# Kernel tuning notes

Measured on AMD Instinct MI355X. Metric: run time of the kernel, lower is better.

## Reference

```python
import jax, jax.numpy as jnp
import numpy as np

N_TRAJ, T, D_DATA, D_LAT, N_UNITS = 8192, 100, 32, 64, 100

def setup_inputs() -> dict:
    key = jax.random.key(0)
    ks = jax.random.split(key, 12)
    w = lambda k, *shape: jax.random.normal(k, shape, jnp.float32) * 0.05
    z = lambda n: jnp.zeros((n,), jnp.float32)
    return {
        "data": jax.random.normal(ks[0], (N_TRAJ, T, D_DATA), jnp.float32),
        "time_steps": jnp.linspace(0.0, 1.0, T, dtype=jnp.float32),  # uniform grid -> dt < interval/50 always
        "prior": jax.random.normal(ks[1], (N_TRAJ, D_LAT), jnp.float32),
        # ODE func MLP: latent -> n_units -> latent
        "Wo1": w(ks[2], D_LAT, N_UNITS), "bo1": z(N_UNITS),
        "Wo2": w(ks[3], N_UNITS, D_LAT), "bo2": z(D_LAT),
        # GRU update/reset/candidate gates, each a 2-layer MLP on concat(y, x)
        "Wz1": w(ks[4], D_LAT + D_DATA, N_UNITS), "bz1": z(N_UNITS),
        "Wz2": w(ks[5], N_UNITS, D_LAT), "bz2": z(D_LAT),
        "Wr1": w(ks[6], D_LAT + D_DATA, N_UNITS), "br1": z(N_UNITS),
        "Wr2": w(ks[7], N_UNITS, D_LAT), "br2": z(D_LAT),
        "Wh1": w(ks[8], D_LAT + D_DATA, N_UNITS), "bh1": z(N_UNITS),
        "Wh2": w(ks[9], N_UNITS, D_LAT), "bh2": z(D_LAT),
    }

def _odernn(data, time_steps, prior,
            Wo1, bo1, Wo2, bo2,
            Wz1, bz1, Wz2, bz2,
            Wr1, br1, Wr2, br2,
            Wh1, bh1, Wh2, bh2):
    # Replicates the original loop's (prev_t, t_i) bookkeeping faithfully:
    # iteration 1 uses dt = ts[1] - ts[0]; after each iteration the code sets
    # prev_t, t_i = ts[i], ts[i-1], so iteration i >= 2 uses dt = ts[i-2] - ts[i-1].
    dts = jnp.concatenate([time_steps[1:2] - time_steps[0:1],
                           time_steps[:-2] - time_steps[1:-1]])  # [T-1]
    xs = jnp.swapaxes(data[:, 1:, :], 0, 1)  # [T-1, N, D_DATA] for scan

    def ode_func(y):  # [N, D_LAT] -> [N, D_LAT]
        return jnp.tanh(y @ Wo1 + bo1) @ Wo2 + bo2

    def gru_update(y, x):  # [N, D_LAT], [N, D_DATA] -> [N, D_LAT]
        yx = jnp.concatenate([y, x], axis=-1)
        zg = jax.nn.sigmoid(jnp.tanh(yx @ Wz1 + bz1) @ Wz2 + bz2)
        rg = jax.nn.sigmoid(jnp.tanh(yx @ Wr1 + br1) @ Wr2 + br2)
        ryx = jnp.concatenate([rg * y, x], axis=-1)
        h = jnp.tanh(jnp.tanh(ryx @ Wh1 + bh1) @ Wh2 + bh2)
        return (1.0 - zg) * h + zg * y

    def step(y, inp):
        dt, x = inp
        # |dt| < minimum_step branch: single explicit-Euler increment
        y_ode = y + ode_func(y) * dt
        return gru_update(y_ode, x), None

    y_final, _ = jax.lax.scan(step, prior, (dts, xs))
    return y_final

def reference(data, time_steps, prior,
              Wo1, bo1, Wo2, bo2,
              Wz1, bz1, Wz2, bz2,
              Wr1, br1, Wr2, br2,
              Wh1, bh1, Wh2, bh2):
    return _odernn(data, time_steps, prior,
                   Wo1, bo1, Wo2, bo2,
                   Wz1, bz1, Wz2, bz2,
                   Wr1, br1, Wr2, br2,
                   Wh1, bh1, Wh2, bh2)
```

## Files before the change

### kernel.cpp

```cpp
#include <hip/hip_runtime.h>

#define T_STEPS 100
#define NTRAJ   8192
#define MBLK    32
#define W_TILES 112
#define W_BYTES (W_TILES * 1024)
#define TILEBUF 22528
#define LDS_TOTAL (W_BYTES + 2 * TILEBUF)

typedef __attribute__((ext_vector_type(8))) _Float16 f16x8;
typedef __attribute__((ext_vector_type(4))) _Float16 f16x4;
typedef __attribute__((ext_vector_type(4))) float    f32x4;

#define MFMA16(a, b, c) __builtin_amdgcn_mfma_f32_16x16x32_f16((a), (b), (c), 0, 0, 0)

#define SWZ(row, col) ((col) ^ (((row) & 7) << 3))

__device__ __forceinline__ float fast_tanh(float x) {
    float e = __expf(2.f * x);
    return 1.f - 2.f * __builtin_amdgcn_rcpf(1.f + e);
}
__device__ __forceinline__ float fast_sigmoid(float x) {
    float e = __expf(-x);
    return __builtin_amdgcn_rcpf(1.f + e);
}

__global__ void pack_kernel(const float* __restrict__ Wo1, const float* __restrict__ Wo2,
                            const float* __restrict__ Wz1, const float* __restrict__ Wz2,
                            const float* __restrict__ Wr1, const float* __restrict__ Wr2,
                            const float* __restrict__ Wh1, const float* __restrict__ Wh2,
                            _Float16* __restrict__ P)
{
    int idx = blockIdx.x * 256 + threadIdx.x;
    if (idx >= 144 * 512) return;
    int tile = idx >> 9;
    int r    = idx & 511;
    int lane = r >> 3, j = r & 7;
    int krel = ((lane >> 4) << 3) + j;
    int c16  = lane & 15;
    float val = 0.f;

    if (tile < 14) {
        int t = tile, nt = t >> 1, kt = t & 1;
        int k = kt * 32 + krel, n = nt * 16 + c16;
        if (k < 64 && n < 100) val = Wo1[k * 100 + n];
    } else if (tile < 30) {
        int t = tile - 14, nt = t >> 2, kt = t & 3;
        int k = kt * 32 + krel, n = nt * 16 + c16;
        if (k < 100) val = Wo2[k * 64 + n];
    } else if (tile < 75) {
        int t = tile - 30, nt = t / 3, kt = t % 3;
        int k = kt * 32 + krel;
        if (nt < 7)      { int n = nt * 16 + c16;        if (n < 100) val = Wz1[k * 100 + n]; }
        else if (nt >= 8){ int n = (nt - 8) * 16 + c16;  if (n < 100) val = Wr1[k * 100 + n]; }
    } else if (tile < 107) {
        int t = tile - 75, gate = t >> 4, rem = t & 15, nt = rem >> 2, kt = rem & 3;
        int k = kt * 32 + krel, n = nt * 16 + c16;
        const float* W = gate ? Wr2 : Wz2;
        if (k < 100) val = W[k * 64 + n];
    } else if (tile < 128) {
        int t = tile - 107, nt = t / 3, kt = t % 3;
        int k = kt * 32 + krel, n = nt * 16 + c16;
        if (n < 100) val = Wh1[k * 100 + n];
    } else {
        int t = tile - 128, nt = t >> 2, kt = t & 3;
        int k = kt * 32 + krel, n = nt * 16 + c16;
        if (k < 100) val = Wh2[k * 64 + n];
    }
    P[idx] = (_Float16)val;
}

__device__ __forceinline__ f16x8 ldsA(const _Float16* buf, int stride, int row, int kcol) {
    return *(const f16x8*)(buf + row * stride + SWZ(row, kcol));
}
__device__ __forceinline__ void st4(_Float16* buf, int stride, int traj, int f0,
                                    float a, float b, float c, float d) {
    f16x4 h = {(_Float16)a, (_Float16)b, (_Float16)c, (_Float16)d};
    *(f16x4*)(buf + traj * stride + SWZ(traj, f0)) = h;
}
__device__ __forceinline__ f32x4 loadBias4(const float* b, int f0, int n) {
    f32x4 v = {0.f, 0.f, 0.f, 0.f};
    #pragma unroll
    for (int r = 0; r < 4; ++r) if (f0 + r < n) v[r] = b[f0 + r];
    return v;
}

__global__ __launch_bounds__(512, 2) void odernn_kernel(
    const float* __restrict__ data, const float* __restrict__ ts,
    const float* __restrict__ prior,
    const float* __restrict__ bo1, const float* __restrict__ bo2,
    const float* __restrict__ bz1, const float* __restrict__ bz2,
    const float* __restrict__ br1, const float* __restrict__ br2,
    const float* __restrict__ bh1, const float* __restrict__ bh2,
    const _Float16* __restrict__ P, float* __restrict__ out)
{
    extern __shared__ __align__(16) char smem[];
    _Float16* W = (_Float16*)smem;

    const int tid  = threadIdx.x;
    const int lane = tid & 63;
    const int wv   = tid >> 6;
    const int tg   = wv >> 2;
    const int wq   = wv & 3;
    const int c16  = lane & 15;
    const int g4   = lane >> 4;
    const int m0b  = blockIdx.x * MBLK;
    const int m0   = m0b + tg * 16;
    const int f0   = wq * 16 + (g4 << 2);
    const f16x8* Pt = (const f16x8*)P;
    const f16x8* Wv = (const f16x8*)W;

    _Float16* base = (_Float16*)(smem + W_BYTES + tg * TILEBUF);
    _Float16* sYb = base;
    _Float16* sYX = base + 1024;
    _Float16* sRX = base + 3072;
    _Float16* sH1 = base + 5120;
    _Float16* sZR = base + 7168;

    {
        f16x8* Wd = (f16x8*)W;
        #pragma unroll
        for (int it = 0; it < 14; ++it) {
            int idx = tid + it * 512;
            int ldst = idx >> 6, l = idx & 63;
            int srct = (ldst < 14) ? ldst : ldst + 16;
            Wd[idx] = Pt[srct * 64 + l];
        }
    }

    f32x4 bo1v[2], bh1v[2], bzrv[4];
    #pragma unroll
    for (int t = 0; t < 2; ++t) {
        int nt = wq + 4 * t;
        f32x4 zo = {0.f,0.f,0.f,0.f};
        if (nt < 7) {
            int ft = nt * 16 + (g4 << 2);
            bo1v[t] = loadBias4(bo1, ft, 100);
            bh1v[t] = loadBias4(bh1, ft, 100);
        } else { bo1v[t] = zo; bh1v[t] = zo; }
    }
    #pragma unroll
    for (int q = 0; q < 4; ++q) {
        int i = wq + 4 * q;
        f32x4 v = {0.f,0.f,0.f,0.f};
        if (i < 14) {
            int bt = (i < 7) ? i : i + 1;
            int ft = bt * 16 + (g4 << 2);
            if (i < 7) v = loadBias4(bz1, ft, 100);
            else       v = loadBias4(br1, ft - 128, 100);
        }
        bzrv[q] = v;
    }
    const f32x4 bo2v = *(const f32x4*)(bo2 + f0);
    const f32x4 bz2v = *(const f32x4*)(bz2 + f0);
    const f32x4 br2v = *(const f32x4*)(br2 + f0);
    const f32x4 bh2v = *(const f32x4*)(bh2 + f0);

    f16x8 Ao2[4], Ah2[4];
    #pragma unroll
    for (int kt = 0; kt < 4; ++kt) {
        Ao2[kt] = Pt[(14 + wq * 4 + kt) * 64 + lane];
        Ah2[kt] = Pt[(128 + wq * 4 + kt) * 64 + lane];
    }

    float y[4], yo[4] = {0,0,0,0}, zg[4] = {0,0,0,0};
    {
        f32x4 pv = *(const f32x4*)(prior + (size_t)(m0 + c16) * 64 + f0);
        #pragma unroll
        for (int r = 0; r < 4; ++r) y[r] = pv[r];
        st4(sYb, 64, c16, f0, y[0], y[1], y[2], y[3]);
    }
    {
        int row32 = tid >> 4, col = 112 + (tid & 15);
        int t = row32 >> 4, r16 = row32 & 15;
        _Float16* h1 = (_Float16*)(smem + W_BYTES + t * TILEBUF) + 5120;
        h1[r16 * 128 + SWZ(r16, col)] = (_Float16)0.f;
    }
    for (int i = tid; i < 2 * 16 * 32; i += 512) {
        int t = i >> 9, rem = i & 511;
        int r16 = rem >> 5, cc = rem & 31;
        int col = (cc < 16) ? (112 + cc) : (224 + cc);
        _Float16* zr = (_Float16*)(smem + W_BYTES + t * TILEBUF) + 7168;
        zr[r16 * 256 + SWZ(r16, col)] = (_Float16)0.f;
    }
    __syncthreads();

    const float t0v = ts[0], t1v = ts[1];

    const int t8 = tid & 255;
    const int rowA = t8 >> 5, xcol = t8 & 31;
    const int rowB = rowA + 8;
    const float* xpA = data + (size_t)(m0 + rowA) * (T_STEPS * 32) + 32 + xcol;
    const float* xpB = data + (size_t)(m0 + rowB) * (T_STEPS * 32) + 32 + xcol;
    const int xswA = rowA * 128 + SWZ(rowA, 64 + xcol);
    const int xswB = rowB * 128 + SWZ(rowB, 64 + xcol);
    float xvA = *xpA, xvB = *xpB;

    #pragma unroll 1
    for (int s = 0; s < T_STEPS - 1; ++s) {
        const float dt = (s == 0) ? (t1v - t0v) : (ts[s - 1] - ts[s]);

        {
            f16x8 b0 = ldsA(sYb, 64, c16, (g4 << 3));
            f16x8 b1 = ldsA(sYb, 64, c16, 32 + (g4 << 3));
            #pragma unroll
            for (int t = 0; t < 2; ++t) {
                int nt = wq + 4 * t;
                if (nt < 7) {
                    f32x4 acc0 = bo1v[t];
                    f32x4 z4 = {0.f, 0.f, 0.f, 0.f};
                    acc0 = MFMA16(Wv[(nt * 2 + 0) * 64 + lane], b0, acc0);
                    f32x4 acc1 = MFMA16(Wv[(nt * 2 + 1) * 64 + lane], b1, z4);
                    int ft = nt * 16 + (g4 << 2);
                    st4(sH1, 128, c16, ft,
                        fast_tanh(acc0[0] + acc1[0]), fast_tanh(acc0[1] + acc1[1]),
                        fast_tanh(acc0[2] + acc1[2]), fast_tanh(acc0[3] + acc1[3]));
                }
            }
        }
        {
            _Float16 a = (_Float16)xvA, b = (_Float16)xvB;
            sYX[xswA] = a; sRX[xswA] = a;
            sYX[xswB] = b; sRX[xswB] = b;
            xpA += 32; xpB += 32;
            if (s < T_STEPS - 2) { xvA = *xpA; xvB = *xpB; }
        }
        __syncthreads();

        {
            f32x4 acc0 = bo2v;
            f32x4 z4 = {0.f, 0.f, 0.f, 0.f};
            acc0 = MFMA16(Ao2[0], ldsA(sH1, 128, c16, 0 * 32 + (g4 << 3)), acc0);
            f32x4 acc1 = MFMA16(Ao2[1], ldsA(sH1, 128, c16, 1 * 32 + (g4 << 3)), z4);
            acc0 = MFMA16(Ao2[2], ldsA(sH1, 128, c16, 2 * 32 + (g4 << 3)), acc0);
            acc1 = MFMA16(Ao2[3], ldsA(sH1, 128, c16, 3 * 32 + (g4 << 3)), acc1);
            #pragma unroll
            for (int r = 0; r < 4; ++r) yo[r] = y[r] + dt * (acc0[r] + acc1[r]);
            st4(sYX, 128, c16, f0, yo[0], yo[1], yo[2], yo[3]);
        }
        __syncthreads();

        {
            f16x8 b0 = ldsA(sYX, 128, c16, 0 * 32 + (g4 << 3));
            f16x8 b1 = ldsA(sYX, 128, c16, 1 * 32 + (g4 << 3));
            f16x8 b2 = ldsA(sYX, 128, c16, 2 * 32 + (g4 << 3));
            #pragma unroll
            for (int q = 0; q < 4; ++q) {
                int i = wq + 4 * q;
                if (i < 14) {
                    int bt = (i < 7) ? i : i + 1;
                    f32x4 acc0 = bzrv[q];
                    f32x4 z4 = {0.f, 0.f, 0.f, 0.f};
                    acc0 = MFMA16(Wv[(14 + bt * 3 + 0) * 64 + lane], b0, acc0);
                    f32x4 acc1 = MFMA16(Wv[(14 + bt * 3 + 1) * 64 + lane], b1, z4);
                    acc0 = MFMA16(Wv[(14 + bt * 3 + 2) * 64 + lane], b2, acc0);
                    int ft = bt * 16 + (g4 << 2);
                    st4(sZR, 256, c16, ft,
                        fast_tanh(acc0[0] + acc1[0]), fast_tanh(acc0[1] + acc1[1]),
                        fast_tanh(acc0[2] + acc1[2]), fast_tanh(acc0[3] + acc1[3]));
                }
            }
        }
        __syncthreads();

        {
            f32x4 accz0 = bz2v, accr0 = br2v;
            f32x4 z4 = {0.f, 0.f, 0.f, 0.f};
            f32x4 accz1 = z4, accr1 = z4;
            accz0 = MFMA16(Wv[(59 + wq * 4 + 0) * 64 + lane], ldsA(sZR, 256, c16, 0 * 32 + (g4 << 3)), accz0);
            accr0 = MFMA16(Wv[(75 + wq * 4 + 0) * 64 + lane], ldsA(sZR, 256, c16, 128 + 0 * 32 + (g4 << 3)), accr0);
            accz1 = MFMA16(Wv[(59 + wq * 4 + 1) * 64 + lane], ldsA(sZR, 256, c16, 1 * 32 + (g4 << 3)), accz1);
            accr1 = MFMA16(Wv[(75 + wq * 4 + 1) * 64 + lane], ldsA(sZR, 256, c16, 128 + 1 * 32 + (g4 << 3)), accr1);
            accz0 = MFMA16(Wv[(59 + wq * 4 + 2) * 64 + lane], ldsA(sZR, 256, c16, 2 * 32 + (g4 << 3)), accz0);
            accr0 = MFMA16(Wv[(75 + wq * 4 + 2) * 64 + lane], ldsA(sZR, 256, c16, 128 + 2 * 32 + (g4 << 3)), accr0);
            accz1 = MFMA16(Wv[(59 + wq * 4 + 3) * 64 + lane], ldsA(sZR, 256, c16, 3 * 32 + (g4 << 3)), accz1);
            accr1 = MFMA16(Wv[(75 + wq * 4 + 3) * 64 + lane], ldsA(sZR, 256, c16, 128 + 3 * 32 + (g4 << 3)), accr1);
            float rv[4];
            #pragma unroll
            for (int r = 0; r < 4; ++r) {
                zg[r] = fast_sigmoid(accz0[r] + accz1[r]);
                rv[r] = fast_sigmoid(accr0[r] + accr1[r]) * yo[r];
            }
            st4(sRX, 128, c16, f0, rv[0], rv[1], rv[2], rv[3]);
        }
        __syncthreads();

        {
            f16x8 b0 = ldsA(sRX, 128, c16, 0 * 32 + (g4 << 3));
            f16x8 b1 = ldsA(sRX, 128, c16, 1 * 32 + (g4 << 3));
            f16x8 b2 = ldsA(sRX, 128, c16, 2 * 32 + (g4 << 3));
            #pragma unroll
            for (int t = 0; t < 2; ++t) {
                int nt = wq + 4 * t;
                if (nt < 7) {
                    f32x4 acc0 = bh1v[t];
                    f32x4 z4 = {0.f, 0.f, 0.f, 0.f};
                    acc0 = MFMA16(Wv[(91 + nt * 3 + 0) * 64 + lane], b0, acc0);
                    f32x4 acc1 = MFMA16(Wv[(91 + nt * 3 + 1) * 64 + lane], b1, z4);
                    acc0 = MFMA16(Wv[(91 + nt * 3 + 2) * 64 + lane], b2, acc0);
                    int ft = nt * 16 + (g4 << 2);
                    st4(sH1, 128, c16, ft,
                        fast_tanh(acc0[0] + acc1[0]), fast_tanh(acc0[1] + acc1[1]),
                        fast_tanh(acc0[2] + acc1[2]), fast_tanh(acc0[3] + acc1[3]));
                }
            }
        }
        __syncthreads();

        {
            f32x4 acc0 = bh2v;
            f32x4 z4 = {0.f, 0.f, 0.f, 0.f};
            acc0 = MFMA16(Ah2[0], ldsA(sH1, 128, c16, 0 * 32 + (g4 << 3)), acc0);
            f32x4 acc1 = MFMA16(Ah2[1], ldsA(sH1, 128, c16, 1 * 32 + (g4 << 3)), z4);
            acc0 = MFMA16(Ah2[2], ldsA(sH1, 128, c16, 2 * 32 + (g4 << 3)), acc0);
            acc1 = MFMA16(Ah2[3], ldsA(sH1, 128, c16, 3 * 32 + (g4 << 3)), acc1);
            #pragma unroll
            for (int r = 0; r < 4; ++r) {
                float h = fast_tanh(acc0[r] + acc1[r]);
                y[r] = (1.f - zg[r]) * h + zg[r] * yo[r];
            }
            st4(sYb, 64, c16, f0, y[0], y[1], y[2], y[3]);
        }
        __syncthreads();
    }

    {
        f32x4 ov = {y[0], y[1], y[2], y[3]};
        *(f32x4*)(out + (size_t)(m0 + c16) * 64 + f0) = ov;
    }
}

extern "C" void kernel_launch(void* const* d_in, const int* in_sizes, int n_in,
                              void* d_out, int out_size, void* d_ws, size_t ws_size,
                              hipStream_t stream) {
    const float* data = (const float*)d_in[0];
    const float* ts   = (const float*)d_in[1];
    const float* prior= (const float*)d_in[2];
    const float* Wo1 = (const float*)d_in[3];  const float* bo1 = (const float*)d_in[4];
    const float* Wo2 = (const float*)d_in[5];  const float* bo2 = (const float*)d_in[6];
    const float* Wz1 = (const float*)d_in[7];  const float* bz1 = (const float*)d_in[8];
    const float* Wz2 = (const float*)d_in[9];  const float* bz2 = (const float*)d_in[10];
    const float* Wr1 = (const float*)d_in[11]; const float* br1 = (const float*)d_in[12];
    const float* Wr2 = (const float*)d_in[13]; const float* br2 = (const float*)d_in[14];
    const float* Wh1 = (const float*)d_in[15]; const float* bh1 = (const float*)d_in[16];
    const float* Wh2 = (const float*)d_in[17]; const float* bh2 = (const float*)d_in[18];
    _Float16* P = (_Float16*)d_ws;
    float* out = (float*)d_out;

    hipFuncSetAttribute((const void*)odernn_kernel,
                        hipFuncAttributeMaxDynamicSharedMemorySize, LDS_TOTAL);

    hipLaunchKernelGGL(pack_kernel, dim3((144 * 512 + 255) / 256), dim3(256), 0, stream,
                       Wo1, Wo2, Wz1, Wz2, Wr1, Wr2, Wh1, Wh2, P);
    hipLaunchKernelGGL(odernn_kernel, dim3(NTRAJ / MBLK), dim3(512), LDS_TOTAL, stream,
                       data, ts, prior, bo1, bo2, bz1, bz2, br1, br2, bh1, bh2, P, out);
}
```

Before: 305.0 us.

## Feed data input as register MFMA fragment and precompute x-projections off critical path

Each lane now loads the next step's 8 data values straight into a register f16 fragment instead of staging them through LDS. The x-contributions to the z/r and h first-layer gates are computed early, during the ODE phase, as MFMA accumulators. The later gate MFMAs then chain from those partial sums and only read the 64-wide y or r*y tile from LDS. This shrinks the LDS tiles and takes one dependent MFMA off each serialized gate stage, at the cost of holding extra accumulator registers across barriers.

```diff
diff --git a/kernel.cpp b/kernel.cpp
--- a/kernel.cpp
+++ b/kernel.cpp
@@ -5,11 +5,12 @@
 #define MBLK    32
 #define W_TILES 112
 #define W_BYTES (W_TILES * 1024)
-#define TILEBUF 22528
+#define TILEBUF 18432
 #define LDS_TOTAL (W_BYTES + 2 * TILEBUF)
 
 typedef __attribute__((ext_vector_type(8))) _Float16 f16x8;
 typedef __attribute__((ext_vector_type(4))) _Float16 f16x4;
+typedef __attribute__((ext_vector_type(2))) __fp16   h16x2;
 typedef __attribute__((ext_vector_type(4))) float    f32x4;
 
 #define MFMA16(a, b, c) __builtin_amdgcn_mfma_f32_16x16x32_f16((a), (b), (c), 0, 0, 0)
@@ -84,6 +85,14 @@
     for (int r = 0; r < 4; ++r) if (f0 + r < n) v[r] = b[f0 + r];
     return v;
 }
+__device__ __forceinline__ f16x8 cvt8(f32x4 a, f32x4 b) {
+    union { h16x2 h2[4]; f16x8 v; } u;
+    u.h2[0] = __builtin_amdgcn_cvt_pkrtz(a[0], a[1]);
+    u.h2[1] = __builtin_amdgcn_cvt_pkrtz(a[2], a[3]);
+    u.h2[2] = __builtin_amdgcn_cvt_pkrtz(b[0], b[1]);
+    u.h2[3] = __builtin_amdgcn_cvt_pkrtz(b[2], b[3]);
+    return u.v;
+}
 
 __global__ __launch_bounds__(512, 2) void odernn_kernel(
     const float* __restrict__ data, const float* __restrict__ ts,
@@ -104,8 +113,7 @@
     const int wq   = wv & 3;
     const int c16  = lane & 15;
     const int g4   = lane >> 4;
-    const int m0b  = blockIdx.x * MBLK;
-    const int m0   = m0b + tg * 16;
+    const int m0   = blockIdx.x * MBLK + tg * 16;
     const int f0   = wq * 16 + (g4 << 2);
     const f16x8* Pt = (const f16x8*)P;
     const f16x8* Wv = (const f16x8*)W;
@@ -113,9 +121,9 @@
     _Float16* base = (_Float16*)(smem + W_BYTES + tg * TILEBUF);
     _Float16* sYb = base;
     _Float16* sYX = base + 1024;
-    _Float16* sRX = base + 3072;
-    _Float16* sH1 = base + 5120;
-    _Float16* sZR = base + 7168;
+    _Float16* sRX = base + 2048;
+    _Float16* sH1 = base + 3072;
+    _Float16* sZR = base + 5120;
 
     {
         f16x8* Wd = (f16x8*)W;
@@ -173,33 +181,35 @@
     {
         int row32 = tid >> 4, col = 112 + (tid & 15);
         int t = row32 >> 4, r16 = row32 & 15;
-        _Float16* h1 = (_Float16*)(smem + W_BYTES + t * TILEBUF) + 5120;
+        _Float16* h1 = (_Float16*)(smem + W_BYTES + t * TILEBUF) + 3072;
         h1[r16 * 128 + SWZ(r16, col)] = (_Float16)0.f;
     }
     for (int i = tid; i < 2 * 16 * 32; i += 512) {
         int t = i >> 9, rem = i & 511;
         int r16 = rem >> 5, cc = rem & 31;
         int col = (cc < 16) ? (112 + cc) : (224 + cc);
-        _Float16* zr = (_Float16*)(smem + W_BYTES + t * TILEBUF) + 7168;
+        _Float16* zr = (_Float16*)(smem + W_BYTES + t * TILEBUF) + 5120;
         zr[r16 * 256 + SWZ(r16, col)] = (_Float16)0.f;
     }
     __syncthreads();
 
     const float t0v = ts[0], t1v = ts[1];
 
-    const int t8 = tid & 255;
-    const int rowA = t8 >> 5, xcol = t8 & 31;
-    const int rowB = rowA + 8;
-    const float* xpA = data + (size_t)(m0 + rowA) * (T_STEPS * 32) + 32 + xcol;
-    const float* xpB = data + (size_t)(m0 + rowB) * (T_STEPS * 32) + 32 + xcol;
-    const int xswA = rowA * 128 + SWZ(rowA, 64 + xcol);
-    const int xswB = rowB * 128 + SWZ(rowB, 64 + xcol);
-    float xvA = *xpA, xvB = *xpB;
+    const float* xptr = data + (size_t)(m0 + c16) * (T_STEPS * 32) + 32 + (g4 << 3);
+    f32x4 xn0 = *(const f32x4*)(xptr);
+    f32x4 xn1 = *(const f32x4*)(xptr + 4);
+    f16x8 xfrag = cvt8(xn0, xn1);
 
     #pragma unroll 1
     for (int s = 0; s < T_STEPS - 1; ++s) {
         const float dt = (s == 0) ? (t1v - t0v) : (ts[s - 1] - ts[s]);
 
+        xptr += 32;
+        if (s < T_STEPS - 2) {
+            xn0 = *(const f32x4*)(xptr);
+            xn1 = *(const f32x4*)(xptr + 4);
+        }
+        f32x4 xacc3[4];
         {
             f16x8 b0 = ldsA(sYb, 64, c16, (g4 << 3));
             f16x8 b1 = ldsA(sYb, 64, c16, 32 + (g4 << 3));
@@ -217,16 +227,18 @@
                         fast_tanh(acc0[2] + acc1[2]), fast_tanh(acc0[3] + acc1[3]));
                 }
             }
-        }
-        {
-            _Float16 a = (_Float16)xvA, b = (_Float16)xvB;
-            sYX[xswA] = a; sRX[xswA] = a;
-            sYX[xswB] = b; sRX[xswB] = b;
-            xpA += 32; xpB += 32;
-            if (s < T_STEPS - 2) { xvA = *xpA; xvB = *xpB; }
-        }
-        __syncthreads();
-
+            #pragma unroll
+            for (int q = 0; q < 4; ++q) {
+                int i = wq + 4 * q;
+                if (i < 14) {
+                    int bt = (i < 7) ? i : i + 1;
+                    xacc3[q] = MFMA16(Wv[(14 + bt * 3 + 2) * 64 + lane], xfrag, bzrv[q]);
+                }
+            }
+        }
+        __syncthreads();
+
+        f32x4 xacc5[2];
         {
             f32x4 acc0 = bo2v;
             f32x4 z4 = {0.f, 0.f, 0.f, 0.f};
@@ -235,29 +247,31 @@
             acc0 = MFMA16(Ao2[2], ldsA(sH1, 128, c16, 2 * 32 + (g4 << 3)), acc0);
             acc1 = MFMA16(Ao2[3], ldsA(sH1, 128, c16, 3 * 32 + (g4 << 3)), acc1);
             #pragma unroll
+            for (int t = 0; t < 2; ++t) {
+                int nt = wq + 4 * t;
+                if (nt < 7)
+                    xacc5[t] = MFMA16(Wv[(91 + nt * 3 + 2) * 64 + lane], xfrag, bh1v[t]);
+            }
+            #pragma unroll
             for (int r = 0; r < 4; ++r) yo[r] = y[r] + dt * (acc0[r] + acc1[r]);
-            st4(sYX, 128, c16, f0, yo[0], yo[1], yo[2], yo[3]);
-        }
-        __syncthreads();
-
-        {
-            f16x8 b0 = ldsA(sYX, 128, c16, 0 * 32 + (g4 << 3));
-            f16x8 b1 = ldsA(sYX, 128, c16, 1 * 32 + (g4 << 3));
-            f16x8 b2 = ldsA(sYX, 128, c16, 2 * 32 + (g4 << 3));
+            st4(sYX, 64, c16, f0, yo[0], yo[1], yo[2], yo[3]);
+        }
+        __syncthreads();
+
+        {
+            f16x8 b0 = ldsA(sYX, 64, c16, (g4 << 3));
+            f16x8 b1 = ldsA(sYX, 64, c16, 32 + (g4 << 3));
             #pragma unroll
             for (int q = 0; q < 4; ++q) {
                 int i = wq + 4 * q;
                 if (i < 14) {
                     int bt = (i < 7) ? i : i + 1;
-                    f32x4 acc0 = bzrv[q];
-                    f32x4 z4 = {0.f, 0.f, 0.f, 0.f};
-                    acc0 = MFMA16(Wv[(14 + bt * 3 + 0) * 64 + lane], b0, acc0);
-                    f32x4 acc1 = MFMA16(Wv[(14 + bt * 3 + 1) * 64 + lane], b1, z4);
-                    acc0 = MFMA16(Wv[(14 + bt * 3 + 2) * 64 + lane], b2, acc0);
+                    f32x4 acc = MFMA16(Wv[(14 + bt * 3 + 0) * 64 + lane], b0, xacc3[q]);
+                    acc = MFMA16(Wv[(14 + bt * 3 + 1) * 64 + lane], b1, acc);
                     int ft = bt * 16 + (g4 << 2);
                     st4(sZR, 256, c16, ft,
-                        fast_tanh(acc0[0] + acc1[0]), fast_tanh(acc0[1] + acc1[1]),
-                        fast_tanh(acc0[2] + acc1[2]), fast_tanh(acc0[3] + acc1[3]));
+                        fast_tanh(acc[0]), fast_tanh(acc[1]),
+                        fast_tanh(acc[2]), fast_tanh(acc[3]));
                 }
             }
         }
@@ -281,27 +295,23 @@
                 zg[r] = fast_sigmoid(accz0[r] + accz1[r]);
                 rv[r] = fast_sigmoid(accr0[r] + accr1[r]) * yo[r];
             }
-            st4(sRX, 128, c16, f0, rv[0], rv[1], rv[2], rv[3]);
-        }
-        __syncthreads();
-
-        {
-            f16x8 b0 = ldsA(sRX, 128, c16, 0 * 32 + (g4 << 3));
-            f16x8 b1 = ldsA(sRX, 128, c16, 1 * 32 + (g4 << 3));
-            f16x8 b2 = ldsA(sRX, 128, c16, 2 * 32 + (g4 << 3));
+            st4(sRX, 64, c16, f0, rv[0], rv[1], rv[2], rv[3]);
+        }
+        __syncthreads();
+
+        {
+            f16x8 b0 = ldsA(sRX, 64, c16, (g4 << 3));
+            f16x8 b1 = ldsA(sRX, 64, c16, 32 + (g4 << 3));
             #pragma unroll
             for (int t = 0; t < 2; ++t) {
                 int nt = wq + 4 * t;
                 if (nt < 7) {
-                    f32x4 acc0 = bh1v[t];
-                    f32x4 z4 = {0.f, 0.f, 0.f, 0.f};
-                    acc0 = MFMA16(Wv[(91 + nt * 3 + 0) * 64 + lane], b0, acc0);
-                    f32x4 acc1 = MFMA16(Wv[(91 + nt * 3 + 1) * 64 + lane], b1, z4);
-                    acc0 = MFMA16(Wv[(91 + nt * 3 + 2) * 64 + lane], b2, acc0);
+                    f32x4 acc = MFMA16(Wv[(91 + nt * 3 + 0) * 64 + lane], b0, xacc5[t]);
+                    acc = MFMA16(Wv[(91 + nt * 3 + 1) * 64 + lane], b1, acc);
                     int ft = nt * 16 + (g4 << 2);
                     st4(sH1, 128, c16, ft,
-                        fast_tanh(acc0[0] + acc1[0]), fast_tanh(acc0[1] + acc1[1]),
-                        fast_tanh(acc0[2] + acc1[2]), fast_tanh(acc0[3] + acc1[3]));
+                        fast_tanh(acc[0]), fast_tanh(acc[1]),
+                        fast_tanh(acc[2]), fast_tanh(acc[3]));
                 }
             }
         }
@@ -322,6 +332,8 @@
             st4(sYb, 64, c16, f0, y[0], y[1], y[2], y[3]);
         }
         __syncthreads();
+
+        xfrag = cvt8(xn0, xn1);
     }
 
     {
@@ -347,8 +359,8 @@
     _Float16* P = (_Float16*)d_ws;
     float* out = (float*)d_out;
 
-    hipFuncSetAttribute((const void*)odernn_kernel,
-                        hipFuncAttributeMaxDynamicSharedMemorySize, LDS_TOTAL);
+    (void)hipFuncSetAttribute((const void*)odernn_kernel,
+                              hipFuncAttributeMaxDynamicSharedMemorySize, LDS_TOTAL);
 
     hipLaunchKernelGGL(pack_kernel, dim3((144 * 512 + 255) / 256), dim3(256), 0, stream,
                        Wo1, Wo2, Wz1, Wz2, Wr1, Wr2, Wh1, Wh2, P);
```

Measured after the change: 298.9 us. -2.0%, faster.
